# Kernel optimization log

Measured on AMD Instinct MI355X. Metric: run time of the kernel, lower is better.

## Reference

```python
import jax, jax.numpy as jnp
import numpy as np

NUM_HEADS = 4
NUM_GROUPS = 32
EPS = 1e-5


def group_norm(x, gamma, beta):
    B, C, H, W = x.shape
    g = x.reshape(B, NUM_GROUPS, C // NUM_GROUPS, H, W)
    mean = g.mean(axis=(2, 3, 4), keepdims=True)
    var = g.var(axis=(2, 3, 4), keepdims=True)
    g = (g - mean) * jax.lax.rsqrt(var + EPS)
    x = g.reshape(B, C, H, W)
    return x * gamma[None, :, None, None] + beta[None, :, None, None]


def setup_inputs() -> dict:
    key = jax.random.key(0)
    ks = jax.random.split(key, 7)
    B, C, H, W = 16, 256, 32, 32
    x = jax.random.normal(ks[0], (B, C, H, W), dtype=jnp.float32)
    gn_gamma = jnp.ones((C,), dtype=jnp.float32)
    gn_beta = jnp.zeros((C,), dtype=jnp.float32)
    s = 1.0 / np.sqrt(C)
    qkv_w = jax.random.normal(ks[1], (3 * C, C), dtype=jnp.float32) * s
    qkv_b = jnp.zeros((3 * C,), dtype=jnp.float32)
    proj_w = jax.random.normal(ks[2], (C, C), dtype=jnp.float32) * s
    proj_b = jnp.zeros((C,), dtype=jnp.float32)
    return {"x": x, "gn_gamma": gn_gamma, "gn_beta": gn_beta,
            "qkv_w": qkv_w, "qkv_b": qkv_b, "proj_w": proj_w, "proj_b": proj_b}


def reference(x, gn_gamma, gn_beta, qkv_w, qkv_b, proj_w, proj_b):
    B, C, H, W = x.shape
    nh = NUM_HEADS
    d = C // nh
    N = H * W

    h = group_norm(x, gn_gamma, gn_beta)
    # 1x1 conv == channel matmul
    qkv = jnp.einsum('bchw,oc->bohw', h, qkv_w) + qkv_b[None, :, None, None]
    qkv = qkv.reshape(B, 3, nh, d, N)
    q, k, v = qkv[:, 0], qkv[:, 1], qkv[:, 2]  # each [B, nh, d, N]

    scale = 1.0 / jnp.sqrt(jnp.asarray(d, dtype=x.dtype))
    attn = jnp.einsum('bhdn,bhdm->bhnm', q, k) * scale  # [B, nh, N, N]
    attn = jax.nn.softmax(attn, axis=-1)
    out = jnp.einsum('bhnm,bhdm->bhdn', attn, v)  # [B, nh, d, N]
    out = out.reshape(B, C, H, W)

    out = jnp.einsum('bchw,oc->bohw', out, proj_w) + proj_b[None, :, None, None]
    return x + out
```

## Files before the change

kernel.cpp:

```cpp
#include <hip/hip_runtime.h>
#include <math.h>

typedef unsigned short u16;
typedef unsigned int u32;
typedef __attribute__((ext_vector_type(8))) short s16x8;
typedef __attribute__((ext_vector_type(4))) float f32x4;

#define NB 16
#define NN 1024
#define GN_EPS 1e-5f

static __device__ __forceinline__ u16 f2bf(float f) {
    union { float f; u32 u; } v; v.f = f;
    return (u16)((v.u + 0x8000u) >> 16);
}
static __device__ __forceinline__ u32 pk2(float a, float b) {
    union { float f; u32 u; } A, B; A.f = a; B.f = b;
    return __builtin_amdgcn_perm(A.u + 0x8000u, B.u + 0x8000u, 0x03020706u);
}

#define GLL16(gp, lp) __builtin_amdgcn_global_load_lds( \
    (const __attribute__((address_space(1))) void*)(const void*)(gp), \
    (__attribute__((address_space(3))) void*)(void*)(lp), 16, 0, 0)

__global__ __launch_bounds__(256) void gn_stats_kernel(
    const float* __restrict__ x, float2* __restrict__ stats)
{
    const int bg = blockIdx.x;
    const int t  = threadIdx.x;
    const float4* xb = (const float4*)(x + (size_t)bg * 8192);
    float s = 0.f, ss = 0.f;
#pragma unroll
    for (int i = 0; i < 8; ++i) {
        float4 f = xb[t + i * 256];
        s  += f.x + f.y + f.z + f.w;
        ss += f.x * f.x + f.y * f.y + f.z * f.z + f.w * f.w;
    }
#pragma unroll
    for (int off = 32; off > 0; off >>= 1) {
        s  += __shfl_down(s, off);
        ss += __shfl_down(ss, off);
    }
    __shared__ float red[8];
    const int wid = t >> 6;
    if ((t & 63) == 0) { red[wid] = s; red[4 + wid] = ss; }
    __syncthreads();
    if (t == 0) {
        float sa = red[0] + red[1] + red[2] + red[3];
        float sb = red[4] + red[5] + red[6] + red[7];
        float mean = sa * (1.0f / 8192.0f);
        float var  = sb * (1.0f / 8192.0f) - mean * mean;
        stats[bg] = make_float2(mean, 1.0f / sqrtf(var + GN_EPS));
    }
}

__global__ __launch_bounds__(256) void wcvt_kernel(
    const float* __restrict__ qkv_w, const float* __restrict__ proj_w,
    u16* __restrict__ wqb, u16* __restrict__ wpb)
{
    int i = blockIdx.x * 256 + threadIdx.x;
    if (i < 49152) {
        float4 f = ((const float4*)qkv_w)[i];
        *(uint2*)(wqb + (size_t)i * 4) = make_uint2(pk2(f.x, f.y), pk2(f.z, f.w));
    } else {
        int j = i - 49152;
        float4 f = ((const float4*)proj_w)[j];
        *(uint2*)(wpb + (size_t)j * 4) = make_uint2(pk2(f.x, f.y), pk2(f.z, f.w));
    }
}

__global__ __launch_bounds__(256) void gnorm_t_kernel(
    const float* __restrict__ x, const float2* __restrict__ stats,
    const float* __restrict__ gamma, const float* __restrict__ beta,
    u16* __restrict__ Xt)
{
    const int b = blockIdx.z, ct = blockIdx.y, nt = blockIdx.x;
    const int t = threadIdx.x;
    __shared__ float T[64][65];
    const float* xb = x + ((size_t)b * 256 + ct * 64) * NN + nt * 64;
#pragma unroll
    for (int i = 0; i < 4; ++i) {
        int row = i * 16 + (t >> 4), col = (t & 15) * 4;
        int ch = ct * 64 + row;
        float2 st = stats[b * 32 + (ch >> 3)];
        float gmv = st.y * gamma[ch];
        float btv = beta[ch] - st.x * gmv;
        float4 f = *(const float4*)&xb[(size_t)row * NN + col];
        T[row][col + 0] = f.x * gmv + btv;
        T[row][col + 1] = f.y * gmv + btv;
        T[row][col + 2] = f.z * gmv + btv;
        T[row][col + 3] = f.w * gmv + btv;
    }
    __syncthreads();
    u16* dst = Xt + ((size_t)b * NN + nt * 64) * 256 + ct * 64;
#pragma unroll
    for (int p = 0; p < 2; ++p) {
        int idx = t + p * 256;
        int nl = idx >> 3, c8 = idx & 7;
        s16x8 pv;
#pragma unroll
        for (int j = 0; j < 8; ++j) pv[j] = (short)f2bf(T[c8 * 8 + j][nl]);
        *(s16x8*)(dst + (size_t)nl * 256 + c8 * 8) = pv;
    }
}

__global__ __launch_bounds__(256) void qkv_mfma_kernel(
    const u16* __restrict__ Wb, const float* __restrict__ bias,
    const u16* __restrict__ Xt,
    u16* __restrict__ qh, u16* __restrict__ kh, u16* __restrict__ vh)
{
    const int b = blockIdx.z, ot = blockIdx.y, nt = blockIdx.x;
    const int t = threadIdx.x, w = t >> 6, l = t & 63;
    const int g = l >> 4, c = l & 15;
    __shared__ u16 Slds[32 * 512];
    const u16* Xb = Xt + ((size_t)b * NN + nt * 128) * 256;
    const u16* Wo = Wb + (size_t)ot * 64 * 256;
    const int part = ot >> 2, h = ot & 3;
    const size_t bhoff = (size_t)(b * 4 + h) << 16;

    if (part < 2) {
#pragma unroll
        for (int s = w; s < 32; s += 4) {
            int osub = s >> 3, ks = s & 7;
            GLL16(Wo + (size_t)(osub * 16 + c) * 256 + ks * 32 + g * 8, Slds + s * 512);
        }
        s16x8 a0[8], a1[8];
#pragma unroll
        for (int ks = 0; ks < 8; ++ks) {
            a0[ks] = *(const s16x8*)(Xb + (size_t)((2 * w) * 16 + c) * 256 + ks * 32 + g * 8);
            a1[ks] = *(const s16x8*)(Xb + (size_t)((2 * w + 1) * 16 + c) * 256 + ks * 32 + g * 8);
        }
        f32x4 acc[2][4];
#pragma unroll
        for (int i = 0; i < 2; ++i)
#pragma unroll
            for (int j = 0; j < 4; ++j) acc[i][j] = (f32x4){0.f, 0.f, 0.f, 0.f};
        __syncthreads();
#pragma unroll
        for (int ks = 0; ks < 8; ++ks)
#pragma unroll
            for (int j = 0; j < 4; ++j) {
                s16x8 bf = *(const s16x8*)(Slds + (j * 8 + ks) * 512 + l * 8);
                acc[0][j] = __builtin_amdgcn_mfma_f32_16x16x32_bf16(a0[ks], bf, acc[0][j], 0, 0, 0);
                acc[1][j] = __builtin_amdgcn_mfma_f32_16x16x32_bf16(a1[ks], bf, acc[1][j], 0, 0, 0);
            }
        const float sc = (part == 0) ? 0.125f : 1.0f;
        float bv[4];
#pragma unroll
        for (int j = 0; j < 4; ++j) bv[j] = bias[ot * 64 + j * 16 + c];
        u16* dst = (part == 0 ? qh : kh) + bhoff + (size_t)(nt * 128) * 64;
#pragma unroll
        for (int i = 0; i < 2; ++i)
#pragma unroll
            for (int j = 0; j < 4; ++j)
#pragma unroll
                for (int r = 0; r < 4; ++r) {
                    int n = (2 * w + i) * 16 + g * 4 + r;
                    dst[(size_t)n * 64 + j * 16 + c] = f2bf((acc[i][j][r] + bv[j]) * sc);
                }
    } else {
        f32x4 acc[8];
#pragma unroll
        for (int j = 0; j < 8; ++j) acc[j] = (f32x4){0.f, 0.f, 0.f, 0.f};
        for (int kk = 0; kk < 256; kk += 128) {
            if (kk) __syncthreads();
#pragma unroll
            for (int s = w; s < 32; s += 4) {
                int nsub = s >> 2, ks = s & 3;
                GLL16(Xb + (size_t)(nsub * 16 + c) * 256 + kk + ks * 32 + g * 8, Slds + s * 512);
            }
            __syncthreads();
#pragma unroll
            for (int ks = 0; ks < 4; ++ks) {
                s16x8 a = *(const s16x8*)(Wo + (size_t)(w * 16 + c) * 256 + kk + ks * 32 + g * 8);
#pragma unroll
                for (int j = 0; j < 8; ++j) {
                    s16x8 xf = *(const s16x8*)(Slds + (j * 4 + ks) * 512 + l * 8);
                    acc[j] = __builtin_amdgcn_mfma_f32_16x16x32_bf16(a, xf, acc[j], 0, 0, 0);
                }
            }
        }
        float bv[4];
#pragma unroll
        for (int r = 0; r < 4; ++r) bv[r] = bias[ot * 64 + w * 16 + g * 4 + r];
        u16* dst = vh + bhoff;
#pragma unroll
        for (int j = 0; j < 8; ++j)
#pragma unroll
            for (int r = 0; r < 4; ++r) {
                int d = w * 16 + g * 4 + r;
                int m = nt * 128 + j * 16 + c;
                dst[(size_t)d * NN + m] = f2bf(acc[j][r] + bv[r]);
            }
    }
}

__global__ __launch_bounds__(512) void attn_mfma_kernel(
    const u16* __restrict__ qh, const u16* __restrict__ kh,
    const u16* __restrict__ vh, u16* __restrict__ aoT)
{
    const int t = threadIdx.x;
    const int w = t >> 6, l = t & 63;
    const int g = l >> 4, c = l & 15;
    const int bid = blockIdx.x;
    const int xcd = bid & 7;
    const int idx = bid >> 3;
    const int qt  = idx & 7;
    const int grp = (idx >> 3) * 8 + xcd;
    const int b = grp >> 2, h = grp & 3;
    const size_t bhoff = (size_t)grp << 16;
    const int n_base = qt * 128 + w * 16;

    __shared__ u16 Klds[2][8 * 512];
    __shared__ u16 Vlds[2][8 * 512];
    __shared__ u16 Plds[8][2 * 512];

    const u16* qb = qh + bhoff;
    const u16* kb = kh + bhoff;
    const u16* vb = vh + bhoff;

    const int msub = w >> 1, uu = w & 1;

    s16x8 qf[2];
#pragma unroll
    for (int u = 0; u < 2; ++u)
        qf[u] = *(const s16x8*)(qb + (size_t)(n_base + c) * 64 + u * 32 + g * 8);

    f32x4 Oacc[4];
    float m_run = -1e30f, l_run = 0.f;
#pragma unroll
    for (int ds = 0; ds < 4; ++ds) Oacc[ds] = (f32x4){0.f, 0.f, 0.f, 0.f};

    u16* pw = &Plds[w][0];

    GLL16(kb + (size_t)(msub * 16 + c) * 64 + uu * 32 + g * 8, &Klds[0][w * 512]);
    GLL16(vb + (size_t)(msub * 16 + c) * NN + uu * 32 + g * 8, &Vlds[0][w * 512]);

    for (int mt = 0; mt < 16; ++mt) {
        const int cur = mt & 1;
        if (mt < 15) {
            const int m1 = (mt + 1) * 64;
            GLL16(kb + (size_t)(m1 + msub * 16 + c) * 64 + uu * 32 + g * 8, &Klds[cur ^ 1][w * 512]);
            GLL16(vb + (size_t)(msub * 16 + c) * NN + m1 + uu * 32 + g * 8, &Vlds[cur ^ 1][w * 512]);
            asm volatile("s_waitcnt vmcnt(2)" ::: "memory");
        } else {
            asm volatile("s_waitcnt vmcnt(0)" ::: "memory");
        }
        __builtin_amdgcn_s_barrier();
        asm volatile("" ::: "memory");

        const u16* Kc = &Klds[cur][0];
        const u16* Vc = &Vlds[cur][0];

        f32x4 S[4];
#pragma unroll
        for (int ms = 0; ms < 4; ++ms) S[ms] = (f32x4){0.f, 0.f, 0.f, 0.f};
#pragma unroll
        for (int ms = 0; ms < 4; ++ms)
#pragma unroll
            for (int u = 0; u < 2; ++u) {
                s16x8 af = *(const s16x8*)(Kc + (ms * 2 + u) * 512 + l * 8);
                S[ms] = __builtin_amdgcn_mfma_f32_16x16x32_bf16(af, qf[u], S[ms], 0, 0, 0);
            }

        s16x8 vf[4][2];
#pragma unroll
        for (int ds = 0; ds < 4; ++ds)
#pragma unroll
            for (int u = 0; u < 2; ++u)
                vf[ds][u] = *(const s16x8*)(Vc + (ds * 2 + u) * 512 + l * 8);

        float tmax = -1e30f;
#pragma unroll
        for (int ms = 0; ms < 4; ++ms)
#pragma unroll
            for (int r = 0; r < 4; ++r) tmax = fmaxf(tmax, S[ms][r]);
        tmax = fmaxf(tmax, __shfl_xor(tmax, 16));
        tmax = fmaxf(tmax, __shfl_xor(tmax, 32));
        if (!__all(tmax <= m_run + 8.f)) {
            float nm  = fmaxf(m_run, tmax);
            float fac = __expf(m_run - nm);
            m_run = nm;
            l_run *= fac;
#pragma unroll
            for (int ds = 0; ds < 4; ++ds)
#pragma unroll
                for (int r = 0; r < 4; ++r) Oacc[ds][r] *= fac;
        }
        const float mm = m_run;
        float rsum = 0.f;
#pragma unroll
        for (int ms = 0; ms < 4; ++ms)
#pragma unroll
            for (int r = 0; r < 4; ++r) {
                float p = __expf(S[ms][r] - mm);
                S[ms][r] = p;
                rsum += p;
            }
        rsum += __shfl_xor(rsum, 16);
        rsum += __shfl_xor(rsum, 32);
        l_run += rsum;
#pragma unroll
        for (int ms = 0; ms < 4; ++ms) {
            u32 d0 = pk2(S[ms][0], S[ms][1]);
            u32 d1 = pk2(S[ms][2], S[ms][3]);
            int off = (ms >> 1) * 512 + ((ms & 1) * 2 + (g >> 1)) * 128 + c * 8 + (g & 1) * 4;
            *(uint2*)(pw + off) = make_uint2(d0, d1);
        }
        asm volatile("s_waitcnt lgkmcnt(0)" ::: "memory");
#pragma unroll
        for (int u = 0; u < 2; ++u) {
            s16x8 pf = *(const s16x8*)(pw + u * 512 + l * 8);
#pragma unroll
            for (int ds = 0; ds < 4; ++ds)
                Oacc[ds] = __builtin_amdgcn_mfma_f32_16x16x32_bf16(vf[ds][u], pf, Oacc[ds], 0, 0, 0);
        }
        asm volatile("" ::: "memory");
        __builtin_amdgcn_s_barrier();
    }

    u16* aob = aoT + (size_t)b * NN * 256 + h * 64;
    float inv = 1.0f / l_run;
    const size_t nrow = (size_t)(n_base + c) * 256;
#pragma unroll
    for (int ds = 0; ds < 4; ++ds) {
        u32 lo = pk2(Oacc[ds][0] * inv, Oacc[ds][1] * inv);
        u32 hi = pk2(Oacc[ds][2] * inv, Oacc[ds][3] * inv);
        *(uint2*)(aob + nrow + ds * 16 + g * 4) = make_uint2(lo, hi);
    }
}

__global__ __launch_bounds__(256) void proj_mfma_kernel(
    const u16* __restrict__ Wb, const float* __restrict__ bias,
    const u16* __restrict__ aoT, const float* __restrict__ x,
    float* __restrict__ out)
{
    const int b = blockIdx.z, ot = blockIdx.y, nt = blockIdx.x;
    const int t = threadIdx.x, w = t >> 6, l = t & 63;
    const int g = l >> 4, c = l & 15;
    __shared__ u16 Slds[32 * 512];
    const u16* Xb = aoT + ((size_t)b * NN + nt * 128) * 256;
    const u16* Wo = Wb + (size_t)ot * 64 * 256;

    f32x4 acc[8];
#pragma unroll
    for (int j = 0; j < 8; ++j) acc[j] = (f32x4){0.f, 0.f, 0.f, 0.f};
    for (int kk = 0; kk < 256; kk += 128) {
        if (kk) __syncthreads();
#pragma unroll
        for (int s = w; s < 32; s += 4) {
            int nsub = s >> 2, ks = s & 3;
            GLL16(Xb + (size_t)(nsub * 16 + c) * 256 + kk + ks * 32 + g * 8, Slds + s * 512);
        }
        __syncthreads();
#pragma unroll
        for (int ks = 0; ks < 4; ++ks) {
            s16x8 a = *(const s16x8*)(Wo + (size_t)(w * 16 + c) * 256 + kk + ks * 32 + g * 8);
#pragma unroll
            for (int j = 0; j < 8; ++j) {
                s16x8 xf = *(const s16x8*)(Slds + (j * 4 + ks) * 512 + l * 8);
                acc[j] = __builtin_amdgcn_mfma_f32_16x16x32_bf16(a, xf, acc[j], 0, 0, 0);
            }
        }
    }
    float bv[4];
#pragma unroll
    for (int r = 0; r < 4; ++r) bv[r] = bias[ot * 64 + w * 16 + g * 4 + r];
#pragma unroll
    for (int j = 0; j < 8; ++j)
#pragma unroll
        for (int r = 0; r < 4; ++r) {
            int o = ot * 64 + w * 16 + g * 4 + r;
            int n = nt * 128 + j * 16 + c;
            size_t addr = ((size_t)b * 256 + o) * NN + n;
            out[addr] = acc[j][r] + bv[r] + x[addr];
        }
}

extern "C" void kernel_launch(void* const* d_in, const int* in_sizes, int n_in,
                              void* d_out, int out_size, void* d_ws, size_t ws_size,
                              hipStream_t stream)
{
    const float* x      = (const float*)d_in[0];
    const float* gamma  = (const float*)d_in[1];
    const float* beta   = (const float*)d_in[2];
    const float* qkv_w  = (const float*)d_in[3];
    const float* qkv_b  = (const float*)d_in[4];
    const float* proj_w = (const float*)d_in[5];
    const float* proj_b = (const float*)d_in[6];
    float* out = (float*)d_out;

    float* ws = (float*)d_ws;
    float2* stats = (float2*)ws;
    u16* Xt  = (u16*)(ws + 1024);
    u16* wqb = Xt + (size_t)4194304;
    u16* wpb = wqb + (size_t)196608;
    u16* qh  = wpb + (size_t)65536;
    u16* kh  = qh + (size_t)4194304;
    u16* vh  = kh + (size_t)4194304;
    u16* aoT = vh + (size_t)4194304;

    gn_stats_kernel<<<dim3(NB * 32), 256, 0, stream>>>(x, stats);
    wcvt_kernel<<<dim3(256), 256, 0, stream>>>(qkv_w, proj_w, wqb, wpb);
    gnorm_t_kernel<<<dim3(16, 4, NB), 256, 0, stream>>>(x, stats, gamma, beta, Xt);

    qkv_mfma_kernel<<<dim3(8, 12, NB), 256, 0, stream>>>(
        wqb, qkv_b, Xt, qh, kh, vh);

    attn_mfma_kernel<<<dim3(512), 512, 0, stream>>>(qh, kh, vh, aoT);

    proj_mfma_kernel<<<dim3(8, 4, NB), 256, 0, stream>>>(
        wpb, proj_b, aoT, x, out);
}
```

Measured before the change: 89.27 us.

## Use 32x32x16 MFMA in attention with register-shuffled P, 4 waves per block

The attention kernel switches from 16x16x32 to 32x32x16 bf16 MFMA tiles, with each wave handling 32 query rows instead of 16 and blocks shrinking from 8 to 4 waves. P no longer goes through LDS: the probabilities are packed into the B-operand layout with cross-half lane shuffles. This aims to cut LDS round-trips and per-row reduction shuffles, and to give each MFMA more work per issue. The cost is fewer waves per block for hiding latency, and each wave now stages two K/V slices.

```diff
diff --git a/kernel.cpp b/kernel.cpp
--- a/kernel.cpp
+++ b/kernel.cpp
@@ -5,6 +5,7 @@
 typedef unsigned int u32;
 typedef __attribute__((ext_vector_type(8))) short s16x8;
 typedef __attribute__((ext_vector_type(4))) float f32x4;
+typedef __attribute__((ext_vector_type(16))) float f32x16;
 
 #define NB 16
 #define NN 1024
@@ -195,13 +196,13 @@
     }
 }
 
-__global__ __launch_bounds__(512) void attn_mfma_kernel(
+__global__ __launch_bounds__(256) void attn_mfma_kernel(
     const u16* __restrict__ qh, const u16* __restrict__ kh,
     const u16* __restrict__ vh, u16* __restrict__ aoT)
 {
     const int t = threadIdx.x;
     const int w = t >> 6, l = t & 63;
-    const int g = l >> 4, c = l & 15;
+    const int lo = l & 31, hi = l >> 5;
     const int bid = blockIdx.x;
     const int xcd = bid & 7;
     const int idx = bid >> 3;
@@ -209,40 +210,42 @@
     const int grp = (idx >> 3) * 8 + xcd;
     const int b = grp >> 2, h = grp & 3;
     const size_t bhoff = (size_t)grp << 16;
-    const int n_base = qt * 128 + w * 16;
+    const int n_base = qt * 128 + w * 32;
 
     __shared__ u16 Klds[2][8 * 512];
     __shared__ u16 Vlds[2][8 * 512];
-    __shared__ u16 Plds[8][2 * 512];
 
     const u16* qb = qh + bhoff;
     const u16* kb = kh + bhoff;
     const u16* vb = vh + bhoff;
 
-    const int msub = w >> 1, uu = w & 1;
-
-    s16x8 qf[2];
-#pragma unroll
-    for (int u = 0; u < 2; ++u)
-        qf[u] = *(const s16x8*)(qb + (size_t)(n_base + c) * 64 + u * 32 + g * 8);
-
-    f32x4 Oacc[4];
+    s16x8 qf[4];
+#pragma unroll
+    for (int ks = 0; ks < 4; ++ks)
+        qf[ks] = *(const s16x8*)(qb + (size_t)(n_base + lo) * 64 + ks * 16 + hi * 8);
+
+    f32x16 Od[2];
+#pragma unroll
+    for (int d = 0; d < 2; ++d)
+#pragma unroll
+        for (int r = 0; r < 16; ++r) Od[d][r] = 0.f;
     float m_run = -1e30f, l_run = 0.f;
-#pragma unroll
-    for (int ds = 0; ds < 4; ++ds) Oacc[ds] = (f32x4){0.f, 0.f, 0.f, 0.f};
-
-    u16* pw = &Plds[w][0];
-
-    GLL16(kb + (size_t)(msub * 16 + c) * 64 + uu * 32 + g * 8, &Klds[0][w * 512]);
-    GLL16(vb + (size_t)(msub * 16 + c) * NN + uu * 32 + g * 8, &Vlds[0][w * 512]);
+
+    const int s0 = 2 * w, s1 = 2 * w + 1;
+
+#define STAGE_K(s, m0v, buf) GLL16(kb + (size_t)((m0v) + ((s) >> 2) * 32 + lo) * 64 + ((s) & 3) * 16 + hi * 8, &Klds[buf][(s) * 512])
+#define STAGE_V(s, m0v, buf) GLL16(vb + (size_t)(((s) >> 2) * 32 + lo) * 1024 + (m0v) + ((s) & 3) * 16 + hi * 8, &Vlds[buf][(s) * 512])
+
+    STAGE_K(s0, 0, 0); STAGE_K(s1, 0, 0);
+    STAGE_V(s0, 0, 0); STAGE_V(s1, 0, 0);
 
     for (int mt = 0; mt < 16; ++mt) {
         const int cur = mt & 1;
         if (mt < 15) {
             const int m1 = (mt + 1) * 64;
-            GLL16(kb + (size_t)(m1 + msub * 16 + c) * 64 + uu * 32 + g * 8, &Klds[cur ^ 1][w * 512]);
-            GLL16(vb + (size_t)(msub * 16 + c) * NN + m1 + uu * 32 + g * 8, &Vlds[cur ^ 1][w * 512]);
-            asm volatile("s_waitcnt vmcnt(2)" ::: "memory");
+            STAGE_K(s0, m1, cur ^ 1); STAGE_K(s1, m1, cur ^ 1);
+            STAGE_V(s0, m1, cur ^ 1); STAGE_V(s1, m1, cur ^ 1);
+            asm volatile("s_waitcnt vmcnt(4)" ::: "memory");
         } else {
             asm volatile("s_waitcnt vmcnt(0)" ::: "memory");
         }
@@ -252,82 +255,89 @@
         const u16* Kc = &Klds[cur][0];
         const u16* Vc = &Vlds[cur][0];
 
-        f32x4 S[4];
-#pragma unroll
-        for (int ms = 0; ms < 4; ++ms) S[ms] = (f32x4){0.f, 0.f, 0.f, 0.f};
-#pragma unroll
-        for (int ms = 0; ms < 4; ++ms)
-#pragma unroll
-            for (int u = 0; u < 2; ++u) {
-                s16x8 af = *(const s16x8*)(Kc + (ms * 2 + u) * 512 + l * 8);
-                S[ms] = __builtin_amdgcn_mfma_f32_16x16x32_bf16(af, qf[u], S[ms], 0, 0, 0);
-            }
-
-        s16x8 vf[4][2];
-#pragma unroll
-        for (int ds = 0; ds < 4; ++ds)
-#pragma unroll
-            for (int u = 0; u < 2; ++u)
-                vf[ds][u] = *(const s16x8*)(Vc + (ds * 2 + u) * 512 + l * 8);
-
-        float tmax = -1e30f;
-#pragma unroll
-        for (int ms = 0; ms < 4; ++ms)
-#pragma unroll
-            for (int r = 0; r < 4; ++r) tmax = fmaxf(tmax, S[ms][r]);
-        tmax = fmaxf(tmax, __shfl_xor(tmax, 16));
+        f32x16 S[2];
+#pragma unroll
+        for (int ms = 0; ms < 2; ++ms)
+#pragma unroll
+            for (int r = 0; r < 16; ++r) S[ms][r] = 0.f;
+#pragma unroll
+        for (int ms = 0; ms < 2; ++ms)
+#pragma unroll
+            for (int ks = 0; ks < 4; ++ks) {
+                s16x8 kf = *(const s16x8*)(Kc + (ms * 4 + ks) * 512 + l * 8);
+                S[ms] = __builtin_amdgcn_mfma_f32_32x32x16_bf16(kf, qf[ks], S[ms], 0, 0, 0);
+            }
+
+        s16x8 vf[2][4];
+#pragma unroll
+        for (int ds = 0; ds < 2; ++ds)
+#pragma unroll
+            for (int ks = 0; ks < 4; ++ks)
+                vf[ds][ks] = *(const s16x8*)(Vc + (ds * 4 + ks) * 512 + l * 8);
+
+        float tmax = S[0][0];
+#pragma unroll
+        for (int ms = 0; ms < 2; ++ms)
+#pragma unroll
+            for (int r = 0; r < 16; ++r) tmax = fmaxf(tmax, S[ms][r]);
         tmax = fmaxf(tmax, __shfl_xor(tmax, 32));
         if (!__all(tmax <= m_run + 8.f)) {
             float nm  = fmaxf(m_run, tmax);
             float fac = __expf(m_run - nm);
-            m_run = nm;
-            l_run *= fac;
-#pragma unroll
-            for (int ds = 0; ds < 4; ++ds)
-#pragma unroll
-                for (int r = 0; r < 4; ++r) Oacc[ds][r] *= fac;
+            m_run = nm; l_run *= fac;
+#pragma unroll
+            for (int d = 0; d < 2; ++d)
+#pragma unroll
+                for (int r = 0; r < 16; ++r) Od[d][r] *= fac;
         }
         const float mm = m_run;
         float rsum = 0.f;
 #pragma unroll
-        for (int ms = 0; ms < 4; ++ms)
-#pragma unroll
-            for (int r = 0; r < 4; ++r) {
+        for (int ms = 0; ms < 2; ++ms)
+#pragma unroll
+            for (int r = 0; r < 16; ++r) {
                 float p = __expf(S[ms][r] - mm);
-                S[ms][r] = p;
-                rsum += p;
-            }
-        rsum += __shfl_xor(rsum, 16);
+                S[ms][r] = p; rsum += p;
+            }
         rsum += __shfl_xor(rsum, 32);
         l_run += rsum;
-#pragma unroll
-        for (int ms = 0; ms < 4; ++ms) {
-            u32 d0 = pk2(S[ms][0], S[ms][1]);
-            u32 d1 = pk2(S[ms][2], S[ms][3]);
-            int off = (ms >> 1) * 512 + ((ms & 1) * 2 + (g >> 1)) * 128 + c * 8 + (g & 1) * 4;
-            *(uint2*)(pw + off) = make_uint2(d0, d1);
-        }
-        asm volatile("s_waitcnt lgkmcnt(0)" ::: "memory");
-#pragma unroll
-        for (int u = 0; u < 2; ++u) {
-            s16x8 pf = *(const s16x8*)(pw + u * 512 + l * 8);
-#pragma unroll
-            for (int ds = 0; ds < 4; ++ds)
-                Oacc[ds] = __builtin_amdgcn_mfma_f32_16x16x32_bf16(vf[ds][u], pf, Oacc[ds], 0, 0, 0);
-        }
+
+#pragma unroll
+        for (int ks = 0; ks < 4; ++ks) {
+            const int ms = ks >> 1, kp = ks & 1;
+            u32 pa0 = pk2(S[ms][8 * kp + 0], S[ms][8 * kp + 1]);
+            u32 pa1 = pk2(S[ms][8 * kp + 2], S[ms][8 * kp + 3]);
+            u32 pb0 = pk2(S[ms][8 * kp + 4], S[ms][8 * kp + 5]);
+            u32 pb1 = pk2(S[ms][8 * kp + 6], S[ms][8 * kp + 7]);
+            u32 xa0 = (u32)__shfl_xor((int)pa0, 32);
+            u32 xa1 = (u32)__shfl_xor((int)pa1, 32);
+            u32 xb0 = (u32)__shfl_xor((int)pb0, 32);
+            u32 xb1 = (u32)__shfl_xor((int)pb1, 32);
+            union { u32 u[4]; s16x8 v; } pf;
+            pf.u[0] = hi ? xb0 : pa0;
+            pf.u[1] = hi ? xb1 : pa1;
+            pf.u[2] = hi ? pb0 : xa0;
+            pf.u[3] = hi ? pb1 : xa1;
+#pragma unroll
+            for (int ds = 0; ds < 2; ++ds)
+                Od[ds] = __builtin_amdgcn_mfma_f32_32x32x16_bf16(vf[ds][ks], pf.v, Od[ds], 0, 0, 0);
+        }
+
         asm volatile("" ::: "memory");
         __builtin_amdgcn_s_barrier();
     }
 
     u16* aob = aoT + (size_t)b * NN * 256 + h * 64;
-    float inv = 1.0f / l_run;
-    const size_t nrow = (size_t)(n_base + c) * 256;
-#pragma unroll
-    for (int ds = 0; ds < 4; ++ds) {
-        u32 lo = pk2(Oacc[ds][0] * inv, Oacc[ds][1] * inv);
-        u32 hi = pk2(Oacc[ds][2] * inv, Oacc[ds][3] * inv);
-        *(uint2*)(aob + nrow + ds * 16 + g * 4) = make_uint2(lo, hi);
-    }
+    const float inv = 1.0f / l_run;
+    const size_t nrow = (size_t)(n_base + lo) * 256;
+#pragma unroll
+    for (int ds = 0; ds < 2; ++ds)
+#pragma unroll
+        for (int q2 = 0; q2 < 4; ++q2) {
+            u32 u0 = pk2(Od[ds][4 * q2 + 0] * inv, Od[ds][4 * q2 + 1] * inv);
+            u32 u1 = pk2(Od[ds][4 * q2 + 2] * inv, Od[ds][4 * q2 + 3] * inv);
+            *(uint2*)(aob + nrow + ds * 32 + 8 * q2 + 4 * hi) = make_uint2(u0, u1);
+        }
 }
 
 __global__ __launch_bounds__(256) void proj_mfma_kernel(
@@ -407,7 +417,7 @@
     qkv_mfma_kernel<<<dim3(8, 12, NB), 256, 0, stream>>>(
         wqb, qkv_b, Xt, qh, kh, vh);
 
-    attn_mfma_kernel<<<dim3(512), 512, 0, stream>>>(qh, kh, vh, aoT);
+    attn_mfma_kernel<<<dim3(512), 256, 0, stream>>>(qh, kh, vh, aoT);
 
     proj_mfma_kernel<<<dim3(8, 4, NB), 256, 0, stream>>>(
         wpb, proj_b, aoT, x, out);
```

New measurement: 93.63 us. 4.9% more time.

## Split attention over key halves with a separate combine kernel

Applied to the files above, without the earlier changes.

Attention is split along the key dimension into two halves, doubling the grid from 512 to 1024 blocks so more workgroups can fill the GPU. Each half writes unnormalized partial outputs and per-row max/sum stats, and a new combine kernel merges them into aoT. The double-buffered K/V prefetch is replaced with a single buffer synchronized by two __syncthreads per tile, which removes load/compute overlap. The row max and sum reductions are also restructured as trees. The cost is an extra kernel launch plus a round-trip of bf16 partials through global memory, and the partials lose some precision from bf16 rounding before the merge.

```diff
diff --git a/kernel.cpp b/kernel.cpp
--- a/kernel.cpp
+++ b/kernel.cpp
@@ -17,6 +17,9 @@
 static __device__ __forceinline__ u32 pk2(float a, float b) {
     union { float f; u32 u; } A, B; A.f = a; B.f = b;
     return __builtin_amdgcn_perm(A.u + 0x8000u, B.u + 0x8000u, 0x03020706u);
+}
+static __device__ __forceinline__ float bf2f(u16 u) {
+    union { u32 u; float f; } v; v.u = (u32)u << 16; return v.f;
 }
 
 #define GLL16(gp, lp) __builtin_amdgcn_global_load_lds( \
@@ -197,22 +200,24 @@
 
 __global__ __launch_bounds__(512) void attn_mfma_kernel(
     const u16* __restrict__ qh, const u16* __restrict__ kh,
-    const u16* __restrict__ vh, u16* __restrict__ aoT)
+    const u16* __restrict__ vh, u16* __restrict__ po,
+    float2* __restrict__ pstat)
 {
     const int t = threadIdx.x;
     const int w = t >> 6, l = t & 63;
     const int g = l >> 4, c = l & 15;
     const int bid = blockIdx.x;
     const int xcd = bid & 7;
-    const int idx = bid >> 3;
-    const int qt  = idx & 7;
-    const int grp = (idx >> 3) * 8 + xcd;
-    const int b = grp >> 2, h = grp & 3;
+    const int r0  = bid >> 3;
+    const int qt  = r0 & 7;
+    const int mh  = (r0 >> 3) & 1;
+    const int grp = (r0 >> 4) * 8 + xcd;
     const size_t bhoff = (size_t)grp << 16;
     const int n_base = qt * 128 + w * 16;
-
-    __shared__ u16 Klds[2][8 * 512];
-    __shared__ u16 Vlds[2][8 * 512];
+    const int m_base = mh * 512;
+
+    __shared__ u16 Klds[8 * 512];
+    __shared__ u16 Vlds[8 * 512];
     __shared__ u16 Plds[8][2 * 512];
 
     const u16* qb = qh + bhoff;
@@ -233,24 +238,12 @@
 
     u16* pw = &Plds[w][0];
 
-    GLL16(kb + (size_t)(msub * 16 + c) * 64 + uu * 32 + g * 8, &Klds[0][w * 512]);
-    GLL16(vb + (size_t)(msub * 16 + c) * NN + uu * 32 + g * 8, &Vlds[0][w * 512]);
-
-    for (int mt = 0; mt < 16; ++mt) {
-        const int cur = mt & 1;
-        if (mt < 15) {
-            const int m1 = (mt + 1) * 64;
-            GLL16(kb + (size_t)(m1 + msub * 16 + c) * 64 + uu * 32 + g * 8, &Klds[cur ^ 1][w * 512]);
-            GLL16(vb + (size_t)(msub * 16 + c) * NN + m1 + uu * 32 + g * 8, &Vlds[cur ^ 1][w * 512]);
-            asm volatile("s_waitcnt vmcnt(2)" ::: "memory");
-        } else {
-            asm volatile("s_waitcnt vmcnt(0)" ::: "memory");
-        }
-        __builtin_amdgcn_s_barrier();
-        asm volatile("" ::: "memory");
-
-        const u16* Kc = &Klds[cur][0];
-        const u16* Vc = &Vlds[cur][0];
+    for (int mt = 0; mt < 8; ++mt) {
+        const int m0 = m_base + mt * 64;
+        __syncthreads();
+        GLL16(kb + (size_t)(m0 + msub * 16 + c) * 64 + uu * 32 + g * 8, Klds + w * 512);
+        GLL16(vb + (size_t)(msub * 16 + c) * NN + m0 + uu * 32 + g * 8, Vlds + w * 512);
+        __syncthreads();
 
         f32x4 S[4];
 #pragma unroll
@@ -259,7 +252,7 @@
         for (int ms = 0; ms < 4; ++ms)
 #pragma unroll
             for (int u = 0; u < 2; ++u) {
-                s16x8 af = *(const s16x8*)(Kc + (ms * 2 + u) * 512 + l * 8);
+                s16x8 af = *(const s16x8*)(Klds + (ms * 2 + u) * 512 + l * 8);
                 S[ms] = __builtin_amdgcn_mfma_f32_16x16x32_bf16(af, qf[u], S[ms], 0, 0, 0);
             }
 
@@ -268,13 +261,18 @@
         for (int ds = 0; ds < 4; ++ds)
 #pragma unroll
             for (int u = 0; u < 2; ++u)
-                vf[ds][u] = *(const s16x8*)(Vc + (ds * 2 + u) * 512 + l * 8);
-
-        float tmax = -1e30f;
-#pragma unroll
-        for (int ms = 0; ms < 4; ++ms)
-#pragma unroll
-            for (int r = 0; r < 4; ++r) tmax = fmaxf(tmax, S[ms][r]);
+                vf[ds][u] = *(const s16x8*)(Vlds + (ds * 2 + u) * 512 + l * 8);
+
+        float mx[8];
+#pragma unroll
+        for (int i = 0; i < 4; ++i) {
+            mx[2 * i]     = fmaxf(S[i][0], S[i][1]);
+            mx[2 * i + 1] = fmaxf(S[i][2], S[i][3]);
+        }
+#pragma unroll
+        for (int i = 0; i < 4; ++i) mx[i] = fmaxf(mx[i], mx[i + 4]);
+        mx[0] = fmaxf(mx[0], mx[2]); mx[1] = fmaxf(mx[1], mx[3]);
+        float tmax = fmaxf(mx[0], mx[1]);
         tmax = fmaxf(tmax, __shfl_xor(tmax, 16));
         tmax = fmaxf(tmax, __shfl_xor(tmax, 32));
         if (!__all(tmax <= m_run + 8.f)) {
@@ -288,18 +286,24 @@
                 for (int r = 0; r < 4; ++r) Oacc[ds][r] *= fac;
         }
         const float mm = m_run;
-        float rsum = 0.f;
 #pragma unroll
         for (int ms = 0; ms < 4; ++ms)
 #pragma unroll
-            for (int r = 0; r < 4; ++r) {
-                float p = __expf(S[ms][r] - mm);
-                S[ms][r] = p;
-                rsum += p;
-            }
+            for (int r = 0; r < 4; ++r) S[ms][r] = __expf(S[ms][r] - mm);
+        float sm[8];
+#pragma unroll
+        for (int i = 0; i < 4; ++i) {
+            sm[2 * i]     = S[i][0] + S[i][1];
+            sm[2 * i + 1] = S[i][2] + S[i][3];
+        }
+#pragma unroll
+        for (int i = 0; i < 4; ++i) sm[i] += sm[i + 4];
+        sm[0] += sm[2]; sm[1] += sm[3];
+        float rsum = sm[0] + sm[1];
         rsum += __shfl_xor(rsum, 16);
         rsum += __shfl_xor(rsum, 32);
         l_run += rsum;
+
 #pragma unroll
         for (int ms = 0; ms < 4; ++ms) {
             u32 d0 = pk2(S[ms][0], S[ms][1]);
@@ -315,19 +319,58 @@
             for (int ds = 0; ds < 4; ++ds)
                 Oacc[ds] = __builtin_amdgcn_mfma_f32_16x16x32_bf16(vf[ds][u], pf, Oacc[ds], 0, 0, 0);
         }
-        asm volatile("" ::: "memory");
-        __builtin_amdgcn_s_barrier();
-    }
-
-    u16* aob = aoT + (size_t)b * NN * 256 + h * 64;
-    float inv = 1.0f / l_run;
-    const size_t nrow = (size_t)(n_base + c) * 256;
+    }
+
+    u16* pob = po + (((size_t)mh * 64 + grp) * NN + n_base + c) * 64;
 #pragma unroll
     for (int ds = 0; ds < 4; ++ds) {
-        u32 lo = pk2(Oacc[ds][0] * inv, Oacc[ds][1] * inv);
-        u32 hi = pk2(Oacc[ds][2] * inv, Oacc[ds][3] * inv);
-        *(uint2*)(aob + nrow + ds * 16 + g * 4) = make_uint2(lo, hi);
-    }
+        u32 u0 = pk2(Oacc[ds][0], Oacc[ds][1]);
+        u32 u1 = pk2(Oacc[ds][2], Oacc[ds][3]);
+        *(uint2*)(pob + ds * 16 + g * 4) = make_uint2(u0, u1);
+    }
+    if (l < 16)
+        pstat[((size_t)mh * 64 + grp) * NN + n_base + c] = make_float2(m_run, l_run);
+}
+
+__global__ __launch_bounds__(256) void attn_combine_kernel(
+    const u16* __restrict__ po, const float2* __restrict__ pstat,
+    u16* __restrict__ aoT)
+{
+    const int bid = blockIdx.x;
+    const int grp = bid >> 4, nt = bid & 15;
+    const int b = grp >> 2, h = grp & 3;
+    const int t = threadIdx.x;
+    const int nn = t >> 2, dq = t & 3;
+    const int n = nt * 64 + nn;
+    const size_t i1 = (size_t)grp * NN + n;
+    float2 s1 = pstat[i1];
+    float2 s2 = pstat[(size_t)64 * NN + i1];
+    float M  = fmaxf(s1.x, s2.x);
+    float w1 = __expf(s1.x - M), w2 = __expf(s2.x - M);
+    float invl = 1.0f / (w1 * s1.y + w2 * s2.y);
+    w1 *= invl; w2 *= invl;
+    const u16* p1 = po + i1 * 64 + dq * 16;
+    const u16* p2 = po + (size_t)4194304 + i1 * 64 + dq * 16;
+    s16x8 a1 = *(const s16x8*)p1;
+    s16x8 a2 = *(const s16x8*)p2;
+    s16x8 b1 = *(const s16x8*)(p1 + 8);
+    s16x8 b2 = *(const s16x8*)(p2 + 8);
+    u16* dst = aoT + ((size_t)b * NN + n) * 256 + h * 64 + dq * 16;
+    u32 o[4];
+#pragma unroll
+    for (int j = 0; j < 4; ++j) {
+        float v0 = w1 * bf2f((u16)a1[2 * j])     + w2 * bf2f((u16)a2[2 * j]);
+        float v1 = w1 * bf2f((u16)a1[2 * j + 1]) + w2 * bf2f((u16)a2[2 * j + 1]);
+        o[j] = pk2(v0, v1);
+    }
+    *(uint4*)dst = make_uint4(o[0], o[1], o[2], o[3]);
+#pragma unroll
+    for (int j = 0; j < 4; ++j) {
+        float v0 = w1 * bf2f((u16)b1[2 * j])     + w2 * bf2f((u16)b2[2 * j]);
+        float v1 = w1 * bf2f((u16)b1[2 * j + 1]) + w2 * bf2f((u16)b2[2 * j + 1]);
+        o[j] = pk2(v0, v1);
+    }
+    *(uint4*)(dst + 8) = make_uint4(o[0], o[1], o[2], o[3]);
 }
 
 __global__ __launch_bounds__(256) void proj_mfma_kernel(
@@ -399,6 +442,8 @@
     u16* kh  = qh + (size_t)4194304;
     u16* vh  = kh + (size_t)4194304;
     u16* aoT = vh + (size_t)4194304;
+    u16* po  = aoT + (size_t)4194304;
+    float2* pstat = (float2*)(po + (size_t)8388608);
 
     gn_stats_kernel<<<dim3(NB * 32), 256, 0, stream>>>(x, stats);
     wcvt_kernel<<<dim3(256), 256, 0, stream>>>(qkv_w, proj_w, wqb, wpb);
@@ -407,7 +452,8 @@
     qkv_mfma_kernel<<<dim3(8, 12, NB), 256, 0, stream>>>(
         wqb, qkv_b, Xt, qh, kh, vh);
 
-    attn_mfma_kernel<<<dim3(512), 512, 0, stream>>>(qh, kh, vh, aoT);
+    attn_mfma_kernel<<<dim3(1024), 512, 0, stream>>>(qh, kh, vh, po, pstat);
+    attn_combine_kernel<<<dim3(1024), 256, 0, stream>>>(po, pstat, aoT);
 
     proj_mfma_kernel<<<dim3(8, 4, NB), 256, 0, stream>>>(
         wpb, proj_b, aoT, x, out);
```

After: 96.58 us. +8.2%, slower.
